# Kernel tuning notes

Measured on AMD Instinct MI355X. Metric: run time of the kernel, lower is better.

Reference implementation:

```python
import jax, jax.numpy as jnp
import numpy as np

N_NODES = 100000
N_EDGES = 1600000
IN_DIM = 128
HID = 64
HEADS = 8
OUTF = HID // HEADS  # out_feats per head = 8
ATTN_SLOPE = 0.2     # DGL GATConv leaky_relu slope for attention logits
ACT_SLOPE = 0.01     # F.leaky_relu default slope for inter-layer activation


def leaky_relu(x, slope):
    return jnp.where(x >= 0, x, slope * x)


def gat_layer(x, src, dst, W, al, ar, b, apply_act):
    # x: [N, Din], W: [Din, H*F], al/ar: [H, F], b: [H*F]
    N = x.shape[0]
    feat = (x @ W).reshape(N, HEADS, OUTF)                     # [N, H, F]
    el = jnp.sum(feat * al[None], axis=-1)                      # [N, H]
    er = jnp.sum(feat * ar[None], axis=-1)                      # [N, H]
    e = leaky_relu(el[src] + er[dst], ATTN_SLOPE)               # [E, H]
    # segment softmax over incoming edges of each dst node
    m = jax.ops.segment_max(e, dst, num_segments=N)             # [N, H]
    ex = jnp.exp(e - m[dst])                                    # [E, H]
    s = jax.ops.segment_sum(ex, dst, num_segments=N)            # [N, H]
    alpha = ex / s[dst]                                         # [E, H]
    msg = feat[src] * alpha[:, :, None]                         # [E, H, F]
    rst = jax.ops.segment_sum(msg, dst, num_segments=N)         # [N, H, F]
    rst = rst + b.reshape(1, HEADS, OUTF)
    if apply_act:
        rst = leaky_relu(rst, ACT_SLOPE)
    return rst.reshape(N, HEADS * OUTF)


def setup_inputs() -> dict:
    key = jax.random.key(0)
    ks = jax.random.split(key, 12)
    n_feat = jax.random.normal(ks[0], (N_NODES, IN_DIM), dtype=jnp.float32)
    src = jax.random.randint(ks[1], (N_EDGES,), 0, N_NODES, dtype=jnp.int32)
    dst = jax.random.randint(ks[2], (N_EDGES,), 0, N_NODES, dtype=jnp.int32)
    sc = 0.1
    W0 = sc * jax.random.normal(ks[3], (IN_DIM, HID), dtype=jnp.float32)
    al0 = sc * jax.random.normal(ks[4], (HEADS, OUTF), dtype=jnp.float32)
    ar0 = sc * jax.random.normal(ks[5], (HEADS, OUTF), dtype=jnp.float32)
    b0 = jnp.zeros((HID,), dtype=jnp.float32)
    W1 = sc * jax.random.normal(ks[6], (HID, HID), dtype=jnp.float32)
    al1 = sc * jax.random.normal(ks[7], (HEADS, OUTF), dtype=jnp.float32)
    ar1 = sc * jax.random.normal(ks[8], (HEADS, OUTF), dtype=jnp.float32)
    b1 = jnp.zeros((HID,), dtype=jnp.float32)
    return {"n_feat": n_feat, "src": src, "dst": dst,
            "W0": W0, "al0": al0, "ar0": ar0, "b0": b0,
            "W1": W1, "al1": al1, "ar1": ar1, "b1": b1}


def reference(n_feat, src, dst, W0, al0, ar0, b0, W1, al1, ar1, b1):
    h = gat_layer(n_feat, src, dst, W0, al0, ar0, b0, apply_act=True)
    h = gat_layer(h, src, dst, W1, al1, ar1, b1, apply_act=False)
    return h
```

## Files before the change

### kernel.cpp

```cpp
#include <hip/hip_runtime.h>
#include <math.h>

#define NN 100000
#define NE 1600000
#define ATTN_SLOPE 0.2f
#define ACT_SLOPE 0.01f

#define NBUK 512
#define BK 196
#define NBLK 256
#define CHUNK ((NE + NBLK - 1) / NBLK)
#define CAP 5120

typedef __attribute__((ext_vector_type(8))) short bf16x8;
typedef __attribute__((ext_vector_type(4))) float f32x4;

__global__ void __launch_bounds__(256) count_kernel(const int* __restrict__ dst,
                                                    int* __restrict__ counts) {
    __shared__ int h[NBUK];
    const int blk = blockIdx.x;
    for (int i = threadIdx.x; i < NBUK; i += 256) h[i] = 0;
    __syncthreads();
    const int beg = blk * CHUNK;
    const int end = (beg + CHUNK < NE) ? beg + CHUNK : NE;
    for (int i = beg + threadIdx.x; i < end; i += 256)
        atomicAdd(&h[dst[i] / BK], 1);
    __syncthreads();
    for (int i = threadIdx.x; i < NBUK; i += 256)
        counts[blk * NBUK + i] = h[i];
}

__global__ void __launch_bounds__(NBLK) scanA(const int* __restrict__ counts,
                                              int* __restrict__ wbase, int* __restrict__ btot) {
    __shared__ int lds[NBLK];
    const int b = blockIdx.x;
    const int t = threadIdx.x;
    const int v = counts[t * NBUK + b];
    lds[t] = v;
    __syncthreads();
    for (int off = 1; off < NBLK; off <<= 1) {
        int u = (t >= off) ? lds[t - off] : 0;
        __syncthreads();
        lds[t] += u;
        __syncthreads();
    }
    wbase[t * NBUK + b] = lds[t] - v;
    if (t == NBLK - 1) btot[b] = lds[t];
}

__global__ void __launch_bounds__(NBUK) scan_bucket(const int* __restrict__ btot,
                                                    int* __restrict__ bbase, int* __restrict__ offs) {
    __shared__ int lds[NBUK];
    const int t = threadIdx.x;
    const int v = btot[t];
    lds[t] = v;
    __syncthreads();
    for (int off = 1; off < NBUK; off <<= 1) {
        int u = (t >= off) ? lds[t - off] : 0;
        __syncthreads();
        lds[t] += u;
        __syncthreads();
    }
    bbase[t] = lds[t] - v;
    if (t == NBUK - 1) { bbase[NBUK] = lds[t]; offs[NN] = lds[t]; }
}

__global__ void __launch_bounds__(256) scatter_radix(const int* __restrict__ src,
                                                     const int* __restrict__ dst,
                                                     const int* __restrict__ wbase,
                                                     const int* __restrict__ bbase,
                                                     int* __restrict__ tmp) {
    __shared__ int base[NBUK];
    __shared__ int cur[NBUK];
    const int blk = blockIdx.x;
    for (int i = threadIdx.x; i < NBUK; i += 256) {
        base[i] = bbase[i] + wbase[blk * NBUK + i];
        cur[i] = 0;
    }
    __syncthreads();
    const int beg = blk * CHUNK;
    const int end = (beg + CHUNK < NE) ? beg + CHUNK : NE;
    for (int i = beg + threadIdx.x; i < end; i += 256) {
        const int d = dst[i];
        const int b = d / BK;
        const int r = atomicAdd(&cur[b], 1);
        tmp[base[b] + r] = (src[i] << 8) | (d - b * BK);
    }
}

__global__ void __launch_bounds__(256) bucket_build(const int* __restrict__ tmp,
                                                    const int* __restrict__ bbase,
                                                    int* __restrict__ offs,
                                                    int* __restrict__ csr_src) {
    __shared__ int epack[CAP];
    __shared__ int csr_loc[CAP];
    __shared__ int cnt[256];
    __shared__ int loff[256];
    const int b = blockIdx.x;
    const int t = threadIdx.x;
    const int ebeg = bbase[b];
    const int nE = bbase[b + 1] - ebeg;
    const int nlo = b * BK;
    const int nn = (nlo < NN) ? ((NN - nlo < BK) ? (NN - nlo) : BK) : 0;
    const bool fits = (nE <= CAP);

    cnt[t] = 0;
    __syncthreads();
    for (int i = t; i < nE; i += 256) {
        const int p = tmp[ebeg + i];
        if (fits) epack[i] = p;
        atomicAdd(&cnt[p & 255], 1);
    }
    __syncthreads();
    const int v = cnt[t];
    for (int off = 1; off < 256; off <<= 1) {
        int u = (t >= off) ? cnt[t - off] : 0;
        __syncthreads();
        cnt[t] += u;
        __syncthreads();
    }
    const int excl = cnt[t] - v;
    loff[t] = excl;
    __syncthreads();
    cnt[t] = 0;
    if (t < nn) offs[nlo + t] = ebeg + excl;
    __syncthreads();
    for (int i = t; i < nE; i += 256) {
        const int p = fits ? epack[i] : tmp[ebeg + i];
        const int dloc = p & 255;
        const int pos = loff[dloc] + atomicAdd(&cnt[dloc], 1);
        if (fits) csr_loc[pos] = p >> 8;
        else csr_src[ebeg + pos] = p >> 8;
    }
    __syncthreads();
    if (fits)
        for (int i = t; i < nE; i += 256) csr_src[ebeg + i] = csr_loc[i];
}

__device__ __forceinline__ unsigned short bfr(float f) {
    unsigned int u = __builtin_bit_cast(unsigned int, f);
    return (unsigned short)((u + 0x7fffu + ((u >> 16) & 1u)) >> 16);
}
__device__ __forceinline__ float bf2f(unsigned short h) {
    return __builtin_bit_cast(float, ((unsigned int)h) << 16);
}
__device__ __forceinline__ float leaky_attn(float e) {
    return fmaf(0.4f, fabsf(e), 0.6f * e);
}

template <int DIN>
__global__ void __launch_bounds__(256) gemm_mfma_kernel(
        const float* __restrict__ x, const float* __restrict__ W,
        const float* __restrict__ al, const float* __restrict__ ar,
        unsigned short* __restrict__ feat, float* __restrict__ el, float* __restrict__ er,
        int nPairTiles) {
    constexpr int KS = DIN / 32;
    const int lane = threadIdx.x & 63;
    const int tw = threadIdx.x >> 6;
    const int colhalf = tw & 1;
    const int l15 = lane & 15;
    const int g = lane >> 4;
    const int colbase = colhalf * 32;

    bf16x8 Bhi[KS][2], Blo[KS][2];
#pragma unroll
    for (int ks = 0; ks < KS; ++ks) {
#pragma unroll
        for (int ct = 0; ct < 2; ++ct) {
            const int col = colbase + ct * 16 + l15;
#pragma unroll
            for (int j = 0; j < 8; ++j) {
                float w = W[(ks * 32 + g * 8 + j) * 64 + col];
                unsigned short h = bfr(w);
                Bhi[ks][ct][j] = (short)h;
                Blo[ks][ct][j] = (short)bfr(w - bf2f(h));
            }
        }
    }
    const float alc0 = al[colbase + l15];
    const float arc0 = ar[colbase + l15];
    const float alc1 = al[colbase + 16 + l15];
    const float arc1 = ar[colbase + 16 + l15];

#pragma unroll 1
    for (int pt = blockIdx.x; pt < nPairTiles; pt += gridDim.x) {
        const int rb = pt * 32 + (tw >> 1) * 16;
        f32x4 acc0 = {0.f, 0.f, 0.f, 0.f};
        f32x4 acc1 = {0.f, 0.f, 0.f, 0.f};
#pragma unroll
        for (int ks = 0; ks < KS; ++ks) {
            const float* xp = x + (size_t)(rb + l15) * DIN + ks * 32 + g * 8;
            f32x4 xa = *(const f32x4*)xp;
            f32x4 xb = *(const f32x4*)(xp + 4);
            bf16x8 Ahi, Alo;
#pragma unroll
            for (int j = 0; j < 4; ++j) {
                unsigned short h = bfr(xa[j]);
                Ahi[j] = (short)h;
                Alo[j] = (short)bfr(xa[j] - bf2f(h));
            }
#pragma unroll
            for (int j = 0; j < 4; ++j) {
                unsigned short h = bfr(xb[j]);
                Ahi[4 + j] = (short)h;
                Alo[4 + j] = (short)bfr(xb[j] - bf2f(h));
            }
            acc0 = __builtin_amdgcn_mfma_f32_16x16x32_bf16(Ahi, Bhi[ks][0], acc0, 0, 0, 0);
            acc0 = __builtin_amdgcn_mfma_f32_16x16x32_bf16(Ahi, Blo[ks][0], acc0, 0, 0, 0);
            acc0 = __builtin_amdgcn_mfma_f32_16x16x32_bf16(Alo, Bhi[ks][0], acc0, 0, 0, 0);
            acc1 = __builtin_amdgcn_mfma_f32_16x16x32_bf16(Ahi, Bhi[ks][1], acc1, 0, 0, 0);
            acc1 = __builtin_amdgcn_mfma_f32_16x16x32_bf16(Ahi, Blo[ks][1], acc1, 0, 0, 0);
            acc1 = __builtin_amdgcn_mfma_f32_16x16x32_bf16(Alo, Bhi[ks][1], acc1, 0, 0, 0);
        }
#pragma unroll
        for (int i = 0; i < 4; ++i) {
            const int n = rb + g * 4 + i;
            feat[(size_t)n * 64 + colbase + l15] = bfr(acc0[i]);
            feat[(size_t)n * 64 + colbase + 16 + l15] = bfr(acc1[i]);
            float vl0 = acc0[i] * alc0, vr0 = acc0[i] * arc0;
            float vl1 = acc1[i] * alc1, vr1 = acc1[i] * arc1;
#pragma unroll
            for (int d = 1; d < 8; d <<= 1) {
                vl0 += __shfl_xor(vl0, d); vr0 += __shfl_xor(vr0, d);
                vl1 += __shfl_xor(vl1, d); vr1 += __shfl_xor(vr1, d);
            }
            if ((lane & 7) == 0) {
                const int hb = (l15 >> 3) & 1;
                const int h0 = colbase / 8;
                el[n * 8 + h0 + hb] = vl0;
                er[n * 8 + h0 + hb] = vr0;
                el[n * 8 + h0 + 2 + hb] = vl1;
                er[n * 8 + h0 + 2 + hb] = vr1;
            }
        }
    }
}

__global__ void __launch_bounds__(128) aggregate_kernel(
        const unsigned short* __restrict__ feat, const float* __restrict__ el,
        const float* __restrict__ er,
        const int* __restrict__ csr_src, const int* __restrict__ offs,
        const float* __restrict__ bias, float* __restrict__ out, int N, int apply_act) {
    const int lane = threadIdx.x & 63;
    int node = (blockIdx.x << 1) + (threadIdx.x >> 6);
    if (node >= N) return;
    node = __builtin_amdgcn_readfirstlane(node);
    const int h = lane >> 3;
    const int beg = __builtin_amdgcn_readfirstlane(offs[node]);
    const int end = __builtin_amdgcn_readfirstlane(offs[node + 1]);
    const float er_n = er[node * 8 + h];

    float s0a = 0.f, s1a = 0.f, a0a = 0.f, a1a = 0.f;
    int k = beg;
    for (; k + 8 <= end; k += 8) {
        int si[8];
        unsigned short fu[8];
        float ev[8];
#pragma unroll
        for (int j = 0; j < 8; ++j) si[j] = csr_src[k + j];
#pragma unroll
        for (int j = 0; j < 8; ++j) fu[j] = feat[(unsigned)(si[j] * 64 + lane)];
#pragma unroll
        for (int j = 0; j < 8; ++j) ev[j] = el[(unsigned)(si[j] * 8 + h)] + er_n;
#pragma unroll
        for (int j = 0; j < 8; ++j) {
            float p = __expf(leaky_attn(ev[j]));
            if (j & 1) { s1a += p; a1a = fmaf(p, bf2f(fu[j]), a1a); }
            else       { s0a += p; a0a = fmaf(p, bf2f(fu[j]), a0a); }
        }
    }
    for (; k + 4 <= end; k += 4) {
        int si[4];
        unsigned short fu[4];
        float ev[4];
#pragma unroll
        for (int j = 0; j < 4; ++j) si[j] = csr_src[k + j];
#pragma unroll
        for (int j = 0; j < 4; ++j) fu[j] = feat[(unsigned)(si[j] * 64 + lane)];
#pragma unroll
        for (int j = 0; j < 4; ++j) ev[j] = el[(unsigned)(si[j] * 8 + h)] + er_n;
#pragma unroll
        for (int j = 0; j < 4; ++j) {
            float p = __expf(leaky_attn(ev[j]));
            if (j & 1) { s1a += p; a1a = fmaf(p, bf2f(fu[j]), a1a); }
            else       { s0a += p; a0a = fmaf(p, bf2f(fu[j]), a0a); }
        }
    }
    for (; k < end; ++k) {
        int sn = csr_src[k];
        unsigned short fv = feat[(unsigned)(sn * 64 + lane)];
        float p = __expf(leaky_attn(el[(unsigned)(sn * 8 + h)] + er_n));
        s0a += p;
        a0a = fmaf(p, bf2f(fv), a0a);
    }

    const float s = s0a + s1a;
    const float acc = a0a + a1a;
    float r = (s > 0.f) ? (acc / s) : 0.f;
    r += bias[lane];
    if (apply_act) r = (r >= 0.f) ? r : ACT_SLOPE * r;
    out[(size_t)node * 64 + lane] = r;
}

extern "C" void kernel_launch(void* const* d_in, const int* in_sizes, int n_in,
                              void* d_out, int out_size, void* d_ws, size_t ws_size,
                              hipStream_t stream) {
    const float* n_feat = (const float*)d_in[0];
    const int*   src    = (const int*)d_in[1];
    const int*   dst    = (const int*)d_in[2];
    const float* W0     = (const float*)d_in[3];
    const float* al0    = (const float*)d_in[4];
    const float* ar0    = (const float*)d_in[5];
    const float* b0     = (const float*)d_in[6];
    const float* W1     = (const float*)d_in[7];
    const float* al1    = (const float*)d_in[8];
    const float* ar1    = (const float*)d_in[9];
    const float* b1     = (const float*)d_in[10];
    float* out = (float*)d_out;

    char* ws = (char*)d_ws;
    size_t off = 0;
    auto alloc = [&](size_t bytes) -> void* {
        void* p = ws + off;
        off += (bytes + 255) & ~(size_t)255;
        return p;
    };
    unsigned short* featA = (unsigned short*)alloc((size_t)NN * 64 * 2);
    float* featB   = (float*)alloc((size_t)NN * 64 * 4);
    float* el      = (float*)alloc((size_t)NN * 8 * 4);
    float* er      = (float*)alloc((size_t)NN * 8 * 4);
    int*   offs    = (int*)alloc((size_t)(NN + 1) * 4);
    int*   csr_src = (int*)alloc((size_t)NE * 4);
    int*   tmp     = (int*)alloc((size_t)NE * 4);
    int*   counts  = (int*)alloc((size_t)NBLK * NBUK * 4);
    int*   wbase   = (int*)alloc((size_t)NBLK * NBUK * 4);
    int*   btot    = (int*)alloc((size_t)NBUK * 4);
    int*   bbase   = (int*)alloc((size_t)(NBUK + 1) * 4);

    count_kernel<<<NBLK, 256, 0, stream>>>(dst, counts);
    scanA<<<NBUK, NBLK, 0, stream>>>(counts, wbase, btot);
    scan_bucket<<<1, NBUK, 0, stream>>>(btot, bbase, offs);
    scatter_radix<<<NBLK, 256, 0, stream>>>(src, dst, wbase, bbase, tmp);
    bucket_build<<<NBUK, 256, 0, stream>>>(tmp, bbase, offs, csr_src);

    const int nPairTiles = NN / 32;

    gemm_mfma_kernel<128><<<nPairTiles, 256, 0, stream>>>(n_feat, W0, al0, ar0, featA, el, er, nPairTiles);
    aggregate_kernel<<<(NN + 1) / 2, 128, 0, stream>>>(featA, el, er, csr_src, offs, b0, featB, NN, 1);

    gemm_mfma_kernel<64><<<nPairTiles, 256, 0, stream>>>(featB, W1, al1, ar1, featA, el, er, nPairTiles);
    aggregate_kernel<<<(NN + 1) / 2, 128, 0, stream>>>(featA, el, er, csr_src, offs, b1, out, NN, 0);
}
```

Measured before the change: 198.4 us.

## Software-pipeline CSR index loads in aggregation and raise bucketing block count

The aggregate kernel now prefetches the next 8 source indices while gathering features and logits for the current 8. Edge tails are handled with clamped indices and zeroed weights instead of separate 4-wide and scalar remainder loops. Separately, the number of blocks used for edge bucketing rises from 256 to 1024, which shrinks the per-block chunk. The predicated tail issues some redundant gathers for nodes whose degree is not a multiple of 8, and the extra blocks add more per-block histogram overhead.

```diff
diff --git a/kernel.cpp b/kernel.cpp
--- a/kernel.cpp
+++ b/kernel.cpp
@@ -8,7 +8,7 @@
 
 #define NBUK 512
 #define BK 196
-#define NBLK 256
+#define NBLK 1024
 #define CHUNK ((NE + NBLK - 1) / NBLK)
 #define CAP 5120
 
@@ -251,47 +251,43 @@
     const float er_n = er[node * 8 + h];
 
     float s0a = 0.f, s1a = 0.f, a0a = 0.f, a1a = 0.f;
-    int k = beg;
-    for (; k + 8 <= end; k += 8) {
+
+    if (beg < end) {
         int si[8];
-        unsigned short fu[8];
-        float ev[8];
-#pragma unroll
-        for (int j = 0; j < 8; ++j) si[j] = csr_src[k + j];
-#pragma unroll
-        for (int j = 0; j < 8; ++j) fu[j] = feat[(unsigned)(si[j] * 64 + lane)];
-#pragma unroll
-        for (int j = 0; j < 8; ++j) ev[j] = el[(unsigned)(si[j] * 8 + h)] + er_n;
 #pragma unroll
         for (int j = 0; j < 8; ++j) {
-            float p = __expf(leaky_attn(ev[j]));
-            if (j & 1) { s1a += p; a1a = fmaf(p, bf2f(fu[j]), a1a); }
-            else       { s0a += p; a0a = fmaf(p, bf2f(fu[j]), a0a); }
-        }
-    }
-    for (; k + 4 <= end; k += 4) {
-        int si[4];
-        unsigned short fu[4];
-        float ev[4];
-#pragma unroll
-        for (int j = 0; j < 4; ++j) si[j] = csr_src[k + j];
-#pragma unroll
-        for (int j = 0; j < 4; ++j) fu[j] = feat[(unsigned)(si[j] * 64 + lane)];
-#pragma unroll
-        for (int j = 0; j < 4; ++j) ev[j] = el[(unsigned)(si[j] * 8 + h)] + er_n;
-#pragma unroll
-        for (int j = 0; j < 4; ++j) {
-            float p = __expf(leaky_attn(ev[j]));
-            if (j & 1) { s1a += p; a1a = fmaf(p, bf2f(fu[j]), a1a); }
-            else       { s0a += p; a0a = fmaf(p, bf2f(fu[j]), a0a); }
-        }
-    }
-    for (; k < end; ++k) {
-        int sn = csr_src[k];
-        unsigned short fv = feat[(unsigned)(sn * 64 + lane)];
-        float p = __expf(leaky_attn(el[(unsigned)(sn * 8 + h)] + er_n));
-        s0a += p;
-        a0a = fmaf(p, bf2f(fv), a0a);
+            const int idx = beg + j;
+            si[j] = csr_src[idx < end ? idx : end - 1];
+        }
+#pragma unroll 1
+        for (int k = beg; k < end; k += 8) {
+            const int kn = k + 8;
+            int sn[8];
+            if (kn < end) {
+#pragma unroll
+                for (int j = 0; j < 8; ++j) {
+                    const int idx = kn + j;
+                    sn[j] = csr_src[idx < end ? idx : end - 1];
+                }
+            }
+            unsigned short fu[8];
+            float ev[8];
+#pragma unroll
+            for (int j = 0; j < 8; ++j) fu[j] = feat[(unsigned)(si[j] * 64 + lane)];
+#pragma unroll
+            for (int j = 0; j < 8; ++j) ev[j] = el[(unsigned)(si[j] * 8 + h)] + er_n;
+#pragma unroll
+            for (int j = 0; j < 8; ++j) {
+                float p = __expf(leaky_attn(ev[j]));
+                p = (k + j < end) ? p : 0.f;
+                if (j & 1) { s1a += p; a1a = fmaf(p, bf2f(fu[j]), a1a); }
+                else       { s0a += p; a0a = fmaf(p, bf2f(fu[j]), a0a); }
+            }
+            if (kn < end) {
+#pragma unroll
+                for (int j = 0; j < 8; ++j) si[j] = sn[j];
+            }
+        }
     }
 
     const float s = s0a + s1a;
```

Result: slower. 211.7 us (+6.7%).
